# Kernel optimization log

Hardware: AMD Instinct MI355X
Metric: run time of the kernel (lower is better)

The kernel has to match this reference:

```python
import jax, jax.numpy as jnp
import numpy as np

TWO_PI = 2.0 * np.pi

def ringify(x):
    # wrap values to [-pi, pi)
    return (x + np.pi) % TWO_PI - np.pi

def complex_mean(x, axes):
    # circular mean direction: atan2(sum sin, sum ringify(cos))
    dir_x = ringify(jnp.cos(x)).sum(axis=axes)
    dir_y = jnp.sin(x).sum(axis=axes)
    return jnp.arctan2(dir_y, dir_x)

def setup_inputs() -> dict:
    key = jax.random.key(0)
    k1, k2, k3, k4 = jax.random.split(key, 4)
    B = 4096
    return {
        "x": jax.random.normal(k1, (B, 1, 28, 28), dtype=jnp.float32),
        "conv1_w": jax.random.normal(k2, (4, 1, 2, 2), dtype=jnp.float32),
        "conv2_w": jax.random.normal(k3, (8, 4, 4, 4), dtype=jnp.float32),
        "ff_w": jax.random.normal(k4, (288, 10), dtype=jnp.float32),
    }

def reference(x, conv1_w, conv2_w, ff_w):
    B = x.shape[0]
    x = ringify(x).reshape(B, 1, 28, 28)

    # --- ring conv1: 2x2 kernel, stride 2 (non-overlapping patches) ---
    # [B,1,28,28] -> [B,14,14,1,2,2]  (matches unfold(2,2,2).unfold(3,2,2).permute)
    p1 = x.reshape(B, 1, 14, 2, 14, 2).transpose(0, 2, 4, 1, 3, 5)
    w1 = conv1_w.transpose(1, 2, 3, 0)            # [1,2,2,4]
    d1 = ringify(p1[..., None] - w1)              # [B,14,14,1,2,2,4]
    h1 = complex_mean(d1, (3, 4, 5))              # [B,14,14,4]

    # --- ring conv2: 4x4 kernel, stride 2 (overlapping patches) ---
    h1 = h1.transpose(0, 3, 1, 2)                 # [B,4,14,14]
    idx = (jnp.arange(6) * 2)[:, None] + jnp.arange(4)[None, :]  # [6,4] window rows/cols
    p2 = h1[:, :, idx, :][:, :, :, :, idx]        # [B,4,6,4,6,4]
    p2 = p2.transpose(0, 2, 4, 1, 3, 5)           # [B,6,6,4,4,4]
    w2 = conv2_w.transpose(1, 2, 3, 0)            # [4,4,4,8]
    d2 = ringify(p2[..., None] - w2)              # [B,6,6,4,4,4,8]
    h2 = complex_mean(d2, (3, 4, 5))              # [B,6,6,8]

    # --- ring feed-forward ---
    f = h2.reshape(B, 288)
    d3 = ringify(f[:, :, None] - ff_w)            # [B,288,10]
    out = complex_mean(d3, (1,))                  # [B,10]
    return jnp.sin(out)
```

## Files before the change

kernel.cpp:

```cpp
#include <hip/hip_runtime.h>
#include <math.h>

#define FFT_OFF 0
#define W2_OFF 2880
#define W1_OFF 3400

typedef float v2f __attribute__((ext_vector_type(2)));

__device__ __forceinline__ v2f shfl_xor_v2(v2f v, int mask) {
    double d = __builtin_bit_cast(double, v);
    d = __shfl_xor(d, mask);
    return __builtin_bit_cast(v2f, d);
}
__device__ __forceinline__ v2f shfl_down_v2(v2f v, int off, int w) {
    double d = __builtin_bit_cast(double, v);
    d = __shfl_down(d, off, w);
    return __builtin_bit_cast(v2f, d);
}

__global__ void precompute_trig(const float* __restrict__ w1,
                                const float* __restrict__ w2,
                                const float* __restrict__ ff,
                                float2* __restrict__ ws) {
    int idx = blockIdx.x * blockDim.x + threadIdx.x;
    if (idx < 2880) {
        int k = idx / 10, n = idx % 10;
        float s, c; sincosf(ff[idx], &s, &c);
        ws[FFT_OFF + n * 288 + k] = make_float2(c, s);
    } else if (idx < 3392) {
        int i = idx - 2880;
        int oc = i >> 6, e = i & 63;
        float s, c; sincosf(w2[i], &s, &c);
        ws[W2_OFF + (oc >> 1) * 130 + e * 2 + (oc & 1)] = make_float2(c, s);
    } else if (idx < 3408) {
        int i = idx - 3392;
        float s, c; sincosf(w1[i], &s, &c);
        ws[W1_OFF + i] = make_float2(c, s);
    }
}

__global__ __launch_bounds__(320) void ringnn_kernel(
    const float* __restrict__ x,
    const float2* __restrict__ ws,
    float* __restrict__ out)
{
    __shared__ __align__(16) float2 trig2[520];
    __shared__ __align__(16) float2 sc1[1008];
    __shared__ __align__(16) float2 sc2[288];
    const int tid = threadIdx.x;
    const float2* __restrict__ fft = ws + FFT_OFF;
    const float2* __restrict__ w1t = ws + W1_OFF;

    int pi = (tid % 196) / 14, pj = tid % 14;
    float2 r0 = make_float2(0.f, 0.f), r1 = make_float2(0.f, 0.f);
    if (tid < 196) {
        const float* xb = x + (size_t)blockIdx.x * 784;
        r0 = *(const float2*)(xb + (2 * pi) * 28 + 2 * pj);
        r1 = *(const float2*)(xb + (2 * pi + 1) * 28 + 2 * pj);
    }

    if (tid < 260) ((float4*)trig2)[tid] = ((const float4*)(ws + W2_OFF))[tid];

    if (tid < 196) {
        float sx[4], cx[4];
        __sincosf(r0.x, &sx[0], &cx[0]);
        __sincosf(r0.y, &sx[1], &cx[1]);
        __sincosf(r1.x, &sx[2], &cx[2]);
        __sincosf(r1.y, &sx[3], &cx[3]);
        #pragma unroll
        for (int oc = 0; oc < 4; oc++) {
            float4 wa = *(const float4*)(w1t + oc * 4);
            float4 wb = *(const float4*)(w1t + oc * 4 + 2);
            v2f A = {0.f, 0.f};
            A = __builtin_elementwise_fma((v2f){-cx[0], sx[0]}, (v2f){wa.y, wa.y}, A);
            A = __builtin_elementwise_fma((v2f){ sx[0], cx[0]}, (v2f){wa.x, wa.x}, A);
            A = __builtin_elementwise_fma((v2f){-cx[1], sx[1]}, (v2f){wa.w, wa.w}, A);
            A = __builtin_elementwise_fma((v2f){ sx[1], cx[1]}, (v2f){wa.z, wa.z}, A);
            A = __builtin_elementwise_fma((v2f){-cx[2], sx[2]}, (v2f){wb.y, wb.y}, A);
            A = __builtin_elementwise_fma((v2f){ sx[2], cx[2]}, (v2f){wb.x, wb.x}, A);
            A = __builtin_elementwise_fma((v2f){-cx[3], sx[3]}, (v2f){wb.w, wb.w}, A);
            A = __builtin_elementwise_fma((v2f){ sx[3], cx[3]}, (v2f){wb.z, wb.z}, A);
            float Y = A.x, X = A.y;
            float inv = rsqrtf(fmaxf(fmaf(X, X, Y * Y), 1e-30f));
            sc1[oc * 252 + pi * 18 + pj] = make_float2(Y * inv, X * inv);
        }
    }
    __syncthreads();

    if (tid < 96) {
        int r = tid;
        int oi = r >> 4, ojg = (r >> 3) & 1, ocp = (r >> 1) & 3, hf = r & 1;
        const float2* wbp = trig2 + ocp * 130;
        v2f a[3][2] = {{{0.f,0.f},{0.f,0.f}},{{0.f,0.f},{0.f,0.f}},{{0.f,0.f},{0.f,0.f}}};
        #pragma unroll
        for (int ch = 0; ch < 4; ch++) {
            #pragma unroll
            for (int kk = 0; kk < 2; kk++) {
                int ki = hf * 2 + kk;
                int base = ch * 252 + (oi * 2 + ki) * 18 + ojg * 6;
                float4 f0 = *(const float4*)(sc1 + base);
                float4 f1 = *(const float4*)(sc1 + base + 2);
                float4 f2 = *(const float4*)(sc1 + base + 4);
                float4 f3 = *(const float4*)(sc1 + base + 6);
                v2f scp[8] = {{f0.x,f0.y},{f0.z,f0.w},{f1.x,f1.y},{f1.z,f1.w},
                              {f2.x,f2.y},{f2.z,f2.w},{f3.x,f3.y},{f3.z,f3.w}};
                int e0 = ch * 16 + ki * 4;
                #pragma unroll
                for (int kj = 0; kj < 4; kj++) {
                    float4 wv = *(const float4*)(wbp + (e0 + kj) * 2);
                    #pragma unroll
                    for (int ojl = 0; ojl < 3; ojl++) {
                        v2f sc = scp[ojl * 2 + kj];
                        v2f msc = {-sc.y, sc.x};
                        a[ojl][0] = __builtin_elementwise_fma(msc, (v2f){wv.y, wv.y}, a[ojl][0]);
                        a[ojl][0] = __builtin_elementwise_fma(sc,  (v2f){wv.x, wv.x}, a[ojl][0]);
                        a[ojl][1] = __builtin_elementwise_fma(msc, (v2f){wv.w, wv.w}, a[ojl][1]);
                        a[ojl][1] = __builtin_elementwise_fma(sc,  (v2f){wv.z, wv.z}, a[ojl][1]);
                    }
                }
            }
        }
        #pragma unroll
        for (int ojl = 0; ojl < 3; ojl++) {
            v2f a0 = a[ojl][0]; a0 += shfl_xor_v2(a[ojl][0], 1);
            v2f a1 = a[ojl][1]; a1 += shfl_xor_v2(a[ojl][1], 1);
            v2f A = hf ? a1 : a0;
            float Y = A.x, X = A.y;
            float inv = rsqrtf(fmaxf(fmaf(X, X, Y * Y), 1e-30f));
            int p = oi * 6 + ojg * 3 + ojl;
            sc2[p * 8 + ocp * 2 + hf] = make_float2(Y * inv, X * inv);
        }
    }
    __syncthreads();

    {
        int n = tid >> 5, s = tid & 31;
        const float2* wn = fft + n * 288;
        v2f A = {0.f, 0.f};
        #pragma unroll
        for (int i = 0; i < 9; i++) {
            int k = i * 32 + s;
            float2 sc = sc2[k];
            float2 w = wn[k];
            A = __builtin_elementwise_fma((v2f){-sc.y, sc.x}, (v2f){w.y, w.y}, A);
            A = __builtin_elementwise_fma((v2f){ sc.x, sc.y}, (v2f){w.x, w.x}, A);
        }
        #pragma unroll
        for (int off = 16; off > 0; off >>= 1)
            A += shfl_down_v2(A, off, 32);
        if (s == 0) {
            float Y = A.x, X = A.y;
            out[(size_t)blockIdx.x * 10 + n] =
                Y * rsqrtf(fmaxf(fmaf(X, X, Y * Y), 1e-30f));
        }
    }
}

extern "C" void kernel_launch(void* const* d_in, const int* in_sizes, int n_in,
                              void* d_out, int out_size, void* d_ws, size_t ws_size,
                              hipStream_t stream) {
    const float* x  = (const float*)d_in[0];
    const float* w1 = (const float*)d_in[1];
    const float* w2 = (const float*)d_in[2];
    const float* ff = (const float*)d_in[3];
    float* out = (float*)d_out;
    const int B = in_sizes[0] / 784;

    float2* ws = (float2*)d_ws;
    precompute_trig<<<14, 256, 0, stream>>>(w1, w2, ff, ws);
    ringnn_kernel<<<B, 320, 0, stream>>>(x, ws, out);
}
```

Before: 86.04 us.

## Run each sample on a single wavefront and drop block barriers

Shrinks the block from 320 threads to one 64-lane wavefront. Each lane now loops over the conv1 positions, conv2 work items and feed-forward outputs that used to be spread across five waves. Both __syncthreads calls are removed, on the assumption that one wave runs in lockstep so its LDS writes are visible to later reads. This cuts barrier overhead, but each block now does its work serially in one wave, and the per-block shared memory allocation caps how many waves a CU can hold. The barrier-free LDS hand-off also relies on the compiler not reordering the cross-lane loads ahead of the stores.

```diff
diff --git a/kernel.cpp b/kernel.cpp
--- a/kernel.cpp
+++ b/kernel.cpp
@@ -39,7 +39,7 @@
     }
 }
 
-__global__ __launch_bounds__(320) void ringnn_kernel(
+__global__ __launch_bounds__(64) void ringnn_kernel(
     const float* __restrict__ x,
     const float2* __restrict__ ws,
     float* __restrict__ out)
@@ -47,94 +47,111 @@
     __shared__ __align__(16) float2 trig2[520];
     __shared__ __align__(16) float2 sc1[1008];
     __shared__ __align__(16) float2 sc2[288];
-    const int tid = threadIdx.x;
+    const int l = threadIdx.x;
     const float2* __restrict__ fft = ws + FFT_OFF;
     const float2* __restrict__ w1t = ws + W1_OFF;
 
-    int pi = (tid % 196) / 14, pj = tid % 14;
-    float2 r0 = make_float2(0.f, 0.f), r1 = make_float2(0.f, 0.f);
-    if (tid < 196) {
-        const float* xb = x + (size_t)blockIdx.x * 784;
-        r0 = *(const float2*)(xb + (2 * pi) * 28 + 2 * pj);
-        r1 = *(const float2*)(xb + (2 * pi + 1) * 28 + 2 * pj);
+    const float* xb = x + (size_t)blockIdx.x * 784;
+    float2 r0[4], r1[4];
+    #pragma unroll
+    for (int r = 0; r < 4; r++) {
+        int pos = r * 64 + l;
+        r0[r] = make_float2(0.f, 0.f); r1[r] = make_float2(0.f, 0.f);
+        if (pos < 196) {
+            int pi = pos / 14, pj = pos % 14;
+            r0[r] = *(const float2*)(xb + (2 * pi) * 28 + 2 * pj);
+            r1[r] = *(const float2*)(xb + (2 * pi + 1) * 28 + 2 * pj);
+        }
     }
 
-    if (tid < 260) ((float4*)trig2)[tid] = ((const float4*)(ws + W2_OFF))[tid];
+    #pragma unroll
+    for (int t = 0; t < 5; t++) {
+        int idx = t * 64 + l;
+        if (idx < 260)
+            ((float4*)trig2)[idx] = ((const float4*)(ws + W2_OFF))[idx];
+    }
 
-    if (tid < 196) {
-        float sx[4], cx[4];
-        __sincosf(r0.x, &sx[0], &cx[0]);
-        __sincosf(r0.y, &sx[1], &cx[1]);
-        __sincosf(r1.x, &sx[2], &cx[2]);
-        __sincosf(r1.y, &sx[3], &cx[3]);
-        #pragma unroll
-        for (int oc = 0; oc < 4; oc++) {
-            float4 wa = *(const float4*)(w1t + oc * 4);
-            float4 wb = *(const float4*)(w1t + oc * 4 + 2);
-            v2f A = {0.f, 0.f};
-            A = __builtin_elementwise_fma((v2f){-cx[0], sx[0]}, (v2f){wa.y, wa.y}, A);
-            A = __builtin_elementwise_fma((v2f){ sx[0], cx[0]}, (v2f){wa.x, wa.x}, A);
-            A = __builtin_elementwise_fma((v2f){-cx[1], sx[1]}, (v2f){wa.w, wa.w}, A);
-            A = __builtin_elementwise_fma((v2f){ sx[1], cx[1]}, (v2f){wa.z, wa.z}, A);
-            A = __builtin_elementwise_fma((v2f){-cx[2], sx[2]}, (v2f){wb.y, wb.y}, A);
-            A = __builtin_elementwise_fma((v2f){ sx[2], cx[2]}, (v2f){wb.x, wb.x}, A);
-            A = __builtin_elementwise_fma((v2f){-cx[3], sx[3]}, (v2f){wb.w, wb.w}, A);
-            A = __builtin_elementwise_fma((v2f){ sx[3], cx[3]}, (v2f){wb.z, wb.z}, A);
-            float Y = A.x, X = A.y;
-            float inv = rsqrtf(fmaxf(fmaf(X, X, Y * Y), 1e-30f));
-            sc1[oc * 252 + pi * 18 + pj] = make_float2(Y * inv, X * inv);
+    #pragma unroll
+    for (int r = 0; r < 4; r++) {
+        int pos = r * 64 + l;
+        if (pos < 196) {
+            int pi = pos / 14, pj = pos % 14;
+            float sx[4], cx[4];
+            __sincosf(r0[r].x, &sx[0], &cx[0]);
+            __sincosf(r0[r].y, &sx[1], &cx[1]);
+            __sincosf(r1[r].x, &sx[2], &cx[2]);
+            __sincosf(r1[r].y, &sx[3], &cx[3]);
+            #pragma unroll
+            for (int oc = 0; oc < 4; oc++) {
+                float4 wa = *(const float4*)(w1t + oc * 4);
+                float4 wb = *(const float4*)(w1t + oc * 4 + 2);
+                v2f A = {0.f, 0.f};
+                A = __builtin_elementwise_fma((v2f){-cx[0], sx[0]}, (v2f){wa.y, wa.y}, A);
+                A = __builtin_elementwise_fma((v2f){ sx[0], cx[0]}, (v2f){wa.x, wa.x}, A);
+                A = __builtin_elementwise_fma((v2f){-cx[1], sx[1]}, (v2f){wa.w, wa.w}, A);
+                A = __builtin_elementwise_fma((v2f){ sx[1], cx[1]}, (v2f){wa.z, wa.z}, A);
+                A = __builtin_elementwise_fma((v2f){-cx[2], sx[2]}, (v2f){wb.y, wb.y}, A);
+                A = __builtin_elementwise_fma((v2f){ sx[2], cx[2]}, (v2f){wb.x, wb.x}, A);
+                A = __builtin_elementwise_fma((v2f){-cx[3], sx[3]}, (v2f){wb.w, wb.w}, A);
+                A = __builtin_elementwise_fma((v2f){ sx[3], cx[3]}, (v2f){wb.z, wb.z}, A);
+                float Y = A.x, X = A.y;
+                float inv = rsqrtf(fmaxf(fmaf(X, X, Y * Y), 1e-30f));
+                sc1[oc * 252 + pi * 18 + pj] = make_float2(Y * inv, X * inv);
+            }
         }
     }
-    __syncthreads();
 
-    if (tid < 96) {
-        int r = tid;
-        int oi = r >> 4, ojg = (r >> 3) & 1, ocp = (r >> 1) & 3, hf = r & 1;
-        const float2* wbp = trig2 + ocp * 130;
-        v2f a[3][2] = {{{0.f,0.f},{0.f,0.f}},{{0.f,0.f},{0.f,0.f}},{{0.f,0.f},{0.f,0.f}}};
-        #pragma unroll
-        for (int ch = 0; ch < 4; ch++) {
+    #pragma unroll
+    for (int rd = 0; rd < 2; rd++) {
+        int item = rd * 64 + l;
+        if (item < 96) {
+            int oi = item >> 4, ojg = (item >> 3) & 1, ocp = (item >> 1) & 3, hf = item & 1;
+            const float2* wbp = trig2 + ocp * 130;
+            v2f a[3][2] = {{{0.f,0.f},{0.f,0.f}},{{0.f,0.f},{0.f,0.f}},{{0.f,0.f},{0.f,0.f}}};
             #pragma unroll
-            for (int kk = 0; kk < 2; kk++) {
-                int ki = hf * 2 + kk;
-                int base = ch * 252 + (oi * 2 + ki) * 18 + ojg * 6;
-                float4 f0 = *(const float4*)(sc1 + base);
-                float4 f1 = *(const float4*)(sc1 + base + 2);
-                float4 f2 = *(const float4*)(sc1 + base + 4);
-                float4 f3 = *(const float4*)(sc1 + base + 6);
-                v2f scp[8] = {{f0.x,f0.y},{f0.z,f0.w},{f1.x,f1.y},{f1.z,f1.w},
-                              {f2.x,f2.y},{f2.z,f2.w},{f3.x,f3.y},{f3.z,f3.w}};
-                int e0 = ch * 16 + ki * 4;
+            for (int ch = 0; ch < 4; ch++) {
                 #pragma unroll
-                for (int kj = 0; kj < 4; kj++) {
-                    float4 wv = *(const float4*)(wbp + (e0 + kj) * 2);
+                for (int kk = 0; kk < 2; kk++) {
+                    int ki = hf * 2 + kk;
+                    int base = ch * 252 + (oi * 2 + ki) * 18 + ojg * 6;
+                    float4 f0 = *(const float4*)(sc1 + base);
+                    float4 f1 = *(const float4*)(sc1 + base + 2);
+                    float4 f2 = *(const float4*)(sc1 + base + 4);
+                    float4 f3 = *(const float4*)(sc1 + base + 6);
+                    v2f scp[8] = {{f0.x,f0.y},{f0.z,f0.w},{f1.x,f1.y},{f1.z,f1.w},
+                                  {f2.x,f2.y},{f2.z,f2.w},{f3.x,f3.y},{f3.z,f3.w}};
+                    int e0 = ch * 16 + ki * 4;
                     #pragma unroll
-                    for (int ojl = 0; ojl < 3; ojl++) {
-                        v2f sc = scp[ojl * 2 + kj];
-                        v2f msc = {-sc.y, sc.x};
-                        a[ojl][0] = __builtin_elementwise_fma(msc, (v2f){wv.y, wv.y}, a[ojl][0]);
-                        a[ojl][0] = __builtin_elementwise_fma(sc,  (v2f){wv.x, wv.x}, a[ojl][0]);
-                        a[ojl][1] = __builtin_elementwise_fma(msc, (v2f){wv.w, wv.w}, a[ojl][1]);
-                        a[ojl][1] = __builtin_elementwise_fma(sc,  (v2f){wv.z, wv.z}, a[ojl][1]);
+                    for (int kj = 0; kj < 4; kj++) {
+                        float4 wv = *(const float4*)(wbp + (e0 + kj) * 2);
+                        #pragma unroll
+                        for (int ojl = 0; ojl < 3; ojl++) {
+                            v2f sc = scp[ojl * 2 + kj];
+                            v2f msc = {-sc.y, sc.x};
+                            a[ojl][0] = __builtin_elementwise_fma(msc, (v2f){wv.y, wv.y}, a[ojl][0]);
+                            a[ojl][0] = __builtin_elementwise_fma(sc,  (v2f){wv.x, wv.x}, a[ojl][0]);
+                            a[ojl][1] = __builtin_elementwise_fma(msc, (v2f){wv.w, wv.w}, a[ojl][1]);
+                            a[ojl][1] = __builtin_elementwise_fma(sc,  (v2f){wv.z, wv.z}, a[ojl][1]);
+                        }
                     }
                 }
             }
-        }
-        #pragma unroll
-        for (int ojl = 0; ojl < 3; ojl++) {
-            v2f a0 = a[ojl][0]; a0 += shfl_xor_v2(a[ojl][0], 1);
-            v2f a1 = a[ojl][1]; a1 += shfl_xor_v2(a[ojl][1], 1);
-            v2f A = hf ? a1 : a0;
-            float Y = A.x, X = A.y;
-            float inv = rsqrtf(fmaxf(fmaf(X, X, Y * Y), 1e-30f));
-            int p = oi * 6 + ojg * 3 + ojl;
-            sc2[p * 8 + ocp * 2 + hf] = make_float2(Y * inv, X * inv);
+            #pragma unroll
+            for (int ojl = 0; ojl < 3; ojl++) {
+                v2f a0 = a[ojl][0]; a0 += shfl_xor_v2(a[ojl][0], 1);
+                v2f a1 = a[ojl][1]; a1 += shfl_xor_v2(a[ojl][1], 1);
+                v2f A = hf ? a1 : a0;
+                float Y = A.x, X = A.y;
+                float inv = rsqrtf(fmaxf(fmaf(X, X, Y * Y), 1e-30f));
+                int p = oi * 6 + ojg * 3 + ojl;
+                sc2[p * 8 + ocp * 2 + hf] = make_float2(Y * inv, X * inv);
+            }
         }
     }
-    __syncthreads();
 
-    {
-        int n = tid >> 5, s = tid & 31;
+    #pragma unroll
+    for (int r = 0; r < 5; r++) {
+        int n = 2 * r + (l >> 5), s = l & 31;
         const float2* wn = fft + n * 288;
         v2f A = {0.f, 0.f};
         #pragma unroll
@@ -168,5 +185,5 @@
 
     float2* ws = (float2*)d_ws;
     precompute_trig<<<14, 256, 0, stream>>>(w1, w2, ff, ws);
-    ringnn_kernel<<<B, 320, 0, stream>>>(x, ws, out);
+    ringnn_kernel<<<B, 64, 0, stream>>>(x, ws, out);
 }
```

Measured after the change: 89.47 us. +4.0%, slower.
